# Kernel tuning notes

Hardware: AMD Instinct MI355X
Metric: run time of the kernel (lower is better)

Reference implementation:

```python
import jax, jax.numpy as jnp
import numpy as np

N_VERTS = 200000
N_TETS = 800000
FREQ_NUM = 4
SCALE = 1.0
HID = 256
D_IN = 3 + 6 * FREQ_NUM  # 27

_TRI_TABLE = np.array([
    [-1,-1,-1,-1,-1,-1],[1,0,2,-1,-1,-1],[4,0,3,-1,-1,-1],[1,4,2,1,3,4],
    [3,1,5,-1,-1,-1],[2,3,0,2,5,3],[1,4,0,1,5,4],[4,2,5,-1,-1,-1],
    [4,5,2,-1,-1,-1],[4,1,0,4,5,1],[3,2,0,3,5,2],[1,3,5,-1,-1,-1],
    [4,1,2,4,3,1],[3,0,4,-1,-1,-1],[2,0,1,-1,-1,-1],[-1,-1,-1,-1,-1,-1]], dtype=np.int32)
_NUM_TRI = np.array([0,1,1,2,1,2,2,1,1,2,2,1,2,1,1,0], dtype=np.int32)
_BASE_EDGES = np.array([0,1,0,2,0,3,1,2,1,3,2,3], dtype=np.int32)


def _pos_enc(x):
    feats = [x]
    for i in range(FREQ_NUM):
        f = float(2 ** i) * np.pi / SCALE
        feats.append(jnp.sin(f * x))
        feats.append(jnp.cos(f * x))
    return jnp.concatenate(feats, axis=-1)  # [N, 27]


def _mlp_sdf(pos, w0, b0, w1, b1, w2, b2, w3, b3, wf, bf):
    h = jax.nn.relu(_pos_enc(pos) @ w0 + b0)
    for w, b in ((w1, b1), (w2, b2), (w3, b3)):
        h = jax.nn.relu(h @ w + b)
    return (h @ wf + bf)[:, 0]  # [N]


def setup_inputs() -> dict:
    key = jax.random.key(0)
    ks = jax.random.split(key, 12)
    def lin(k, fan_in, shape):
        return jax.random.normal(k, shape, jnp.float32) * (2.0 / fan_in) ** 0.5
    return {
        "pos": jax.random.normal(ks[0], (N_VERTS, 3), jnp.float32),
        "tet_fx4": jax.random.randint(ks[1], (N_TETS, 4), 0, N_VERTS, dtype=jnp.int32),
        "w0": lin(ks[2], D_IN, (D_IN, HID)), "b0": jnp.zeros((HID,), jnp.float32),
        "w1": lin(ks[3], HID, (HID, HID)), "b1": jnp.zeros((HID,), jnp.float32),
        "w2": lin(ks[4], HID, (HID, HID)), "b2": jnp.zeros((HID,), jnp.float32),
        "w3": lin(ks[5], HID, (HID, HID)), "b3": jnp.zeros((HID,), jnp.float32),
        "wf": lin(ks[6], HID, (HID, 1)), "bf": jnp.zeros((1,), jnp.float32),
    }


def reference(pos, tet_fx4, w0, b0, w1, b1, w2, b2, w3, b3, wf, bf):
    # SDF from the positional-encoding MLP (DMTetGeometry)
    sdf = _mlp_sdf(pos, w0, b0, w1, b1, w2, b2, w3, b3, wf, bf)

    # --- marching tetrahedra (DMTet.__call__) ---
    occ = sdf > 0                       # [N]
    occ_fx4 = occ[tet_fx4]              # [F,4]
    occ_sum = occ_fx4.sum(-1)
    valid = (occ_sum > 0) & (occ_sum < 4)
    vt = tet_fx4[valid]                 # [V,4] tets crossed by the surface
    occ_v = occ_fx4[valid]              # [V,4]

    # all 6 edges per valid tet, sorted so (lo, hi)
    e = vt[:, _BASE_EDGES].reshape(-1, 2)                         # [6V,2]
    e = jnp.stack([jnp.minimum(e[:, 0], e[:, 1]),
                   jnp.maximum(e[:, 0], e[:, 1])], axis=1)
    uniq, inv = jnp.unique(e, axis=0, return_inverse=True)        # dedup edges
    inv = inv.reshape(-1)

    # edges whose endpoints straddle the zero level set
    cross = occ[uniq].sum(-1) == 1                                 # [U]
    mapping = jnp.where(cross, jnp.cumsum(cross) - 1, -1)          # compact ids
    idx_map = mapping[inv].reshape(-1, 6)                          # [V,6]
    interp_v = uniq[cross]                                         # [M,2]

    # linear interpolation of crossing vertices along each crossing edge
    p = pos[interp_v]                                              # [M,2,3]
    s = sdf[interp_v]                                              # [M,2]
    denom = s[:, 0] - s[:, 1]                                      # s0 + (-s1)
    verts = (p[:, 0] * (-s[:, 1])[:, None] + p[:, 1] * s[:, 0][:, None]) / denom[:, None]

    # triangle table lookup
    tetindex = (occ_v.astype(jnp.int32) * (2 ** jnp.arange(4, dtype=jnp.int32))).sum(-1)
    ntri = jnp.asarray(_NUM_TRI)[tetindex]
    tri = jnp.asarray(_TRI_TABLE)[tetindex]
    m1 = ntri == 1
    m2 = ntri == 2
    f1 = jnp.take_along_axis(idx_map[m1], tri[m1][:, :3], axis=1).reshape(-1, 3)
    f2 = jnp.take_along_axis(idx_map[m2], tri[m2][:, :6], axis=1).reshape(-1, 3)
    faces = jnp.concatenate([f1, f2], axis=0)
    return verts, faces
```

## Files before the change

### kernel.cpp

```cpp
#include <hip/hip_runtime.h>
#include <cstdint>
#include <cstddef>

#define NV 200000
#define NT 800000
#define ROWS 64
#define MAINB 3072
#define TAILB 212
#define MBLK (MAINB+TAILB)
#define NBLK 3125
#define NSEGS 196
#define PCAP 4096

typedef unsigned int u32;
typedef unsigned long long u64;

typedef __attribute__((ext_vector_type(8))) _Float16 half8;
typedef __attribute__((ext_vector_type(4))) float f32x4;
#define MFMA16F __builtin_amdgcn_mfma_f32_16x16x32_f16

__constant__ int c_tri[16][6] = {
  {-1,-1,-1,-1,-1,-1},{1,0,2,-1,-1,-1},{4,0,3,-1,-1,-1},{1,4,2,1,3,4},
  {3,1,5,-1,-1,-1},{2,3,0,2,5,3},{1,4,0,1,5,4},{4,2,5,-1,-1,-1},
  {4,5,2,-1,-1,-1},{4,1,0,4,5,1},{3,2,0,3,5,2},{1,3,5,-1,-1,-1},
  {4,1,2,4,3,1},{3,0,4,-1,-1,-1},{2,0,1,-1,-1,-1},{-1,-1,-1,-1,-1,-1}};
__constant__ int c_ntri[16] = {0,1,1,2,1,2,2,1,1,2,2,1,2,1,1,0};
__constant__ int c_be[12] = {0,1,0,2,0,3,1,2,1,3,2,3};

__device__ __forceinline__ void split2(float x, _Float16& h, _Float16& m){
  h = (_Float16)x;
  const float r = x - (float)h;
  m = (_Float16)(r * 2048.0f);
}

__global__ void split_weights(const float* __restrict__ w0, const float* __restrict__ w1,
                              const float* __restrict__ w2, const float* __restrict__ w3,
                              _Float16* __restrict__ wp, u32* __restrict__ segcur)
{
  const int idx = blockIdx.x*256 + threadIdx.x;
  if (idx < 256) segcur[idx] = 0u;
  int base, k, n, psz;
  float val;
  if (idx < 8192){
    base = 0; psz = 8192; k = idx >> 8; n = idx & 255;
    val = (k < 27) ? w0[k*256 + n] : 0.f;
  } else {
    int r = idx - 8192;
    const int l = r >> 16;
    r &= 65535;
    k = r >> 8; n = r & 255; psz = 65536;
    base = 16384 + l*131072;
    const float* w = (l==0) ? w1 : (l==1) ? w2 : w3;
    val = w[k*256 + n];
  }
  _Float16 h, m; split2(val, h, m);
  const int c = k >> 5, kk = k & 31;
  const int off = (c*256 + n)*32 + kk;
  wp[base + off] = h;
  wp[base + psz + off] = m;
}

template<int MT, int NC, bool LAST>
__device__ __forceinline__ void layer_run(
    const _Float16* __restrict__ Wl, const float* __restrict__ Bv,
    const float* __restrict__ wfv,
    _Float16* __restrict__ Af, float (*part)[8],
    int lane, int wv)
{
  const int l15 = lane & 15, q = lane >> 4;
  const int col0 = wv * 32;
  constexpr u32 PSTl = (u32)(MT*16*264);
  f32x4 g0[MT][2], g1[MT][2];
#pragma unroll
  for (int i=0;i<MT;i++)
#pragma unroll
    for (int j=0;j<2;j++){ g0[i][j] = (f32x4){0.f,0.f,0.f,0.f}; g1[i][j] = (f32x4){0.f,0.f,0.f,0.f}; }

  const _Float16* bp = Wl + (u32)((col0 + l15)*32 + q*8);
  half8 bA[2][2], bB[2][2];

  auto loadB = [&](int c, half8 (*dst)[2]){
#pragma unroll
    for (int p=0;p<2;p++)
#pragma unroll
      for (int nt=0;nt<2;nt++)
        dst[p][nt] = *(const half8*)(bp + (p*NC + c)*8192 + nt*512);
  };
  auto compute = [&](int c, const half8 (*bb)[2]){
#pragma unroll
    for (int mt=0;mt<MT;mt++){
      const _Float16* ap = Af + (u32)((mt*16 + l15)*264 + c*32 + q*8);
      const half8 ah = *(const half8*)(ap);
      const half8 am = *(const half8*)(ap + PSTl);
#pragma unroll
      for (int nt=0;nt<2;nt++){
        g0[mt][nt] = MFMA16F(ah, bb[0][nt], g0[mt][nt], 0,0,0);
        g1[mt][nt] = MFMA16F(ah, bb[1][nt], g1[mt][nt], 0,0,0);
        g1[mt][nt] = MFMA16F(am, bb[0][nt], g1[mt][nt], 0,0,0);
      }
    }
  };

  loadB(0, bA);
  if (NC == 1){
    compute(0, bA);
  } else {
#pragma unroll 1
    for (int ch=0; ch<NC/2; ch++){
      const int c0 = 2*ch;
      loadB(c0+1, bB);
      compute(c0, bA);
      if (c0+2 < NC) loadB(c0+2, bA);
      compute(c0+1, bB);
    }
  }
  __syncthreads();

  const float S = 4.8828125e-4f;
  if (!LAST){
#pragma unroll
    for (int nt=0;nt<2;nt++){
      const int col = col0 + nt*16 + l15;
      const float bias = Bv[col];
#pragma unroll
      for (int mt=0;mt<MT;mt++)
#pragma unroll
        for (int reg=0;reg<4;reg++){
          const int row = mt*16 + q*4 + reg;
          const float v = fmaxf(g0[mt][nt][reg] + S*g1[mt][nt][reg] + bias, 0.f);
          _Float16 h,m; split2(v,h,m);
          Af[(u32)(row*264 + col)] = h;
          Af[PSTl + (u32)(row*264 + col)] = m;
        }
    }
  } else {
    float pr[MT][4];
#pragma unroll
    for (int mt=0;mt<MT;mt++)
#pragma unroll
      for (int reg=0;reg<4;reg++) pr[mt][reg] = 0.f;
#pragma unroll
    for (int nt=0;nt<2;nt++){
      const int col = col0 + nt*16 + l15;
      const float bias = Bv[col];
      const float w = wfv[col];
#pragma unroll
      for (int mt=0;mt<MT;mt++)
#pragma unroll
        for (int reg=0;reg<4;reg++)
          pr[mt][reg] += fmaxf(g0[mt][nt][reg] + S*g1[mt][nt][reg] + bias, 0.f) * w;
    }
#pragma unroll
    for (int s=1;s<16;s<<=1)
#pragma unroll
      for (int mt=0;mt<MT;mt++)
#pragma unroll
        for (int reg=0;reg<4;reg++)
          pr[mt][reg] += __shfl_xor(pr[mt][reg], s, 64);
    if (l15 == 0){
#pragma unroll
      for (int mt=0;mt<MT;mt++)
#pragma unroll
        for (int reg=0;reg<4;reg++)
          part[mt*16 + q*4 + reg][wv] = pr[mt][reg];
    }
  }
  __syncthreads();
}

__device__ __forceinline__ float posenc_val(const float* __restrict__ pos, int gr, int f){
  if (f < 3) return pos[gr*3 + f];
  if (f < 27){
    const int g = (f-3)/6, rem = (f-3)%6;
    const int d = rem % 3;
    const float x = pos[gr*3 + d];
    const float fr = (float)(1 << g) * 3.14159265358979323846f;
    return (rem < 3) ? sinf(fr*x) : cosf(fr*x);
  }
  return 0.f;
}

__global__ __launch_bounds__(512,4) void mlp_mfma(
    const float* __restrict__ pos, const _Float16* __restrict__ wp,
    const float* __restrict__ b0, const float* __restrict__ b1,
    const float* __restrict__ b2, const float* __restrict__ b3,
    const float* __restrict__ wf, const float* __restrict__ bf,
    float* __restrict__ sdf)
{
  __shared__ _Float16 Af[2*ROWS*264];
  __shared__ float part[ROWS][8];
  const int tid = threadIdx.x;
  const int lane = tid & 63, wv = tid >> 6;
  const int bid = blockIdx.x;

  if (bid < MAINB){
    const int row0 = bid * ROWS;
#pragma unroll
    for (int it=0; it<4; it++){
      const int idx = it*512 + tid;
      const int r = idx & 63, f = idx >> 6;
      const float val = posenc_val(pos, row0 + r, f);
      _Float16 h,m; split2(val,h,m);
      Af[(u32)(r*264 + f)] = h;
      Af[(u32)(ROWS*264 + r*264 + f)] = m;
    }
    __syncthreads();

    layer_run<4,1,false>(wp + 0,      b0, nullptr, Af, part, lane, wv);
    layer_run<4,8,false>(wp + 16384,  b1, nullptr, Af, part, lane, wv);
    layer_run<4,8,false>(wp + 147456, b2, nullptr, Af, part, lane, wv);
    layer_run<4,8,true >(wp + 278528, b3, wf,      Af, part, lane, wv);

    if (tid < ROWS){
      float s = 0.f;
#pragma unroll
      for (int w=0; w<8; w++) s += part[tid][w];
      sdf[row0 + tid] = s + bf[0];
    }
  } else {
    const int row0 = MAINB*ROWS + (bid - MAINB) * 16;
    {
      const int r = tid & 15, f = tid >> 4;
      const float val = posenc_val(pos, row0 + r, f);
      _Float16 h,m; split2(val,h,m);
      Af[(u32)(r*264 + f)] = h;
      Af[(u32)(16*264 + r*264 + f)] = m;
    }
    __syncthreads();

    layer_run<1,1,false>(wp + 0,      b0, nullptr, Af, part, lane, wv);
    layer_run<1,8,false>(wp + 16384,  b1, nullptr, Af, part, lane, wv);
    layer_run<1,8,false>(wp + 147456, b2, nullptr, Af, part, lane, wv);
    layer_run<1,8,true >(wp + 278528, b3, wf,      Af, part, lane, wv);

    if (tid < 16){
      float s = 0.f;
#pragma unroll
      for (int w=0; w<8; w++) s += part[tid][w];
      sdf[row0 + tid] = s + bf[0];
    }
  }
}

__device__ __forceinline__ u32 wave_scan_incl(u32 v, int lane){
#pragma unroll
  for (int s=1;s<64;s<<=1){
    const u32 y = __shfl_up(v, s, 64);
    if (lane >= s) v += y;
  }
  return v;
}
__device__ __forceinline__ u32 block_scan_fast(u32 v, u32* sh4, int tid){
  const int lane = tid & 63, wv = tid >> 6;
  const u32 incl = wave_scan_incl(v, lane);
  if (lane == 63) sh4[wv] = incl;
  __syncthreads();
  u32 base = 0;
#pragma unroll
  for (int w=0;w<3;w++) if (w < wv) base += sh4[w];
  return incl + base;
}
__device__ __forceinline__ u64 bscan_u64(u64 v, u64* sh, int tid){
  sh[tid]=v; __syncthreads();
#pragma unroll
  for (int s=1;s<256;s<<=1){
    const u64 y = (tid>=s) ? sh[tid-s] : 0ull;
    __syncthreads();
    sh[tid] += y;
    __syncthreads();
  }
  return sh[tid];
}

__global__ void tet_pairs(const int* __restrict__ tet, const float* __restrict__ sdf,
    unsigned char* __restrict__ codes, u32* __restrict__ tscan, u32* __restrict__ tsum,
    u32* __restrict__ segcur, u64* __restrict__ pairs)
{
  __shared__ u32 sh4[4];
  const int tid = threadIdx.x;
  const int t = blockIdx.x*256 + tid;
  const int4 v = *(const int4*)(&tet[4*t]);
  const int o0 = sdf[v.x] > 0.f;
  const int o1 = sdf[v.y] > 0.f;
  const int o2 = sdf[v.z] > 0.f;
  const int o3 = sdf[v.w] > 0.f;
  const int code = o0 | (o1<<1) | (o2<<2) | (o3<<3);
  codes[t] = (unsigned char)code;
  const int nt = c_ntri[code];
  if (nt > 0){
    const int vv[4] = {v.x, v.y, v.z, v.w};
    const int oc[4] = {o0,o1,o2,o3};
#pragma unroll
    for (int e=0;e<6;e++){
      const int ia = c_be[2*e], ib = c_be[2*e+1];
      if (oc[ia] != oc[ib]){
        const int p = vv[ia], q = vv[ib];
        const int lo = p<q ? p : q, hi = p<q ? q : p;
        const int seg = lo >> 10;
        const u32 slot = atomicAdd(&segcur[seg], 1u);
        if (slot < PCAP)
          pairs[(size_t)seg*PCAP + slot] = ((u64)(u32)lo << 32) | (u32)hi;
      }
    }
  }
  const u32 my = (u32)(nt==1) | ((u32)(nt==2)<<16);
  const u32 incl = block_scan_fast(my, sh4, tid);
  tscan[t] = incl - my;
  if (tid == 255) tsum[blockIdx.x] = incl;
}

__global__ void seg_process(const u64* __restrict__ pairs_in, const u32* __restrict__ segcur,
    u64* __restrict__ uq, u32* __restrict__ ucnt, u32* __restrict__ ucnt_ex,
    u32* __restrict__ usum, const u32* __restrict__ tsum, u64* __restrict__ tsumE,
    u32* __restrict__ meta)
{
  const int tid = threadIdx.x;
  if (blockIdx.x == NSEGS){
    __shared__ u64 sh64[256];
    u64 loc[13]; u64 tot = 0ull;
#pragma unroll
    for (int i=0;i<13;i++){
      const int idx = tid*13 + i;
      const u32 p = (idx < NBLK) ? tsum[idx] : 0u;
      const u64 u = (u64)(p & 0xffffu) | ((u64)(p >> 16) << 32);
      loc[i] = u; tot += u;
    }
    const u64 incl = bscan_u64(tot, sh64, tid);
    u64 run = incl - tot;
#pragma unroll
    for (int i=0;i<13;i++){
      const int idx = tid*13 + i;
      if (idx < NBLK) tsumE[idx] = run;
      run += loc[i];
    }
    if (tid == 255){ meta[0] = (u32)(incl & 0xffffffffull); meta[1] = (u32)(incl >> 32); }
    return;
  }

  __shared__ u64 P[PCAP];
  __shared__ u32 sh4[4];
  __shared__ u32 shbase;
  const int seg = blockIdx.x;
  int n = (int)segcur[seg];
  if (n > PCAP) n = PCAP;
  int np = 1; while (np < n) np <<= 1;

  for (int i=tid; i<np; i+=256)
    P[i] = (i < n) ? pairs_in[(size_t)seg*PCAP + i] : ~0ull;
  if (tid == 0) shbase = 0u;
  __syncthreads();

  for (int k=2; k<=np; k<<=1){
    for (int j=k>>1; j>0; j>>=1){
      for (int i=tid; i<np; i+=256){
        const int ij = i ^ j;
        if (ij > i){
          const u64 a = P[i], b = P[ij];
          const bool up = ((i & k) == 0);
          if ((a > b) == up){ P[i] = b; P[ij] = a; }
        }
      }
      __syncthreads();
    }
  }

  for (int c=0; c<n; c+=256){
    const int i = c + tid;
    u64 key = 0ull; u32 f = 0u;
    if (i < n){
      key = P[i];
      f = (i == 0 || P[i] != P[i-1]) ? 1u : 0u;
    }
    __syncthreads();
    const u32 incl = block_scan_fast(f, sh4, tid);
    const u32 base = shbase;
    if (f) P[base + incl - 1u] = key;
    __syncthreads();
    if (tid == 255) shbase = base + incl;
    __syncthreads();
  }
  const int uc = (int)shbase;

  for (int i=tid; i<uc; i+=256) uq[(size_t)seg*PCAP + i] = P[i];

  const int lo0 = seg << 10;
  for (int c=0; c<1024; c+=256){
    const int lo = lo0 + c + tid;
    if (lo < NV){
      const u64 kl = (u64)(u32)lo << 32;
      const u64 kh = (u64)(u32)(lo+1) << 32;
      int a=0, b=uc;
      while (a < b){ const int m=(a+b)>>1; if (P[m] < kl) a=m+1; else b=m; }
      const int lb = a;
      b = uc;
      while (a < b){ const int m=(a+b)>>1; if (P[m] < kh) a=m+1; else b=m; }
      ucnt_ex[lo] = (u32)lb;
      ucnt[lo] = (u32)(a - lb);
    }
  }
  if (tid == 0) usum[seg] = (u32)uc;
}

__global__ void emit_all(const int* __restrict__ tet, const float* __restrict__ pos,
    const float* __restrict__ sdf, const unsigned char* __restrict__ codes,
    const u32* __restrict__ tscan, const u64* __restrict__ tsumE, const u32* __restrict__ meta,
    const u64* __restrict__ uq, const u32* __restrict__ ucnt, const u32* __restrict__ ucnt_ex,
    const u32* __restrict__ usum, float* __restrict__ out, int out_size)
{
  __shared__ u32 sh4[4];
  __shared__ u32 shu[NSEGS];
  __shared__ u32 shM;
  const int tid = threadIdx.x;
  {
    const u32 v = (tid < NSEGS) ? usum[tid] : 0u;
    const u32 incl = block_scan_fast(v, sh4, tid);
    if (tid < NSEGS) shu[tid] = incl - v;
    if (tid == NSEGS-1) shM = incl;
    __syncthreads();
  }

  if (blockIdx.x < NSEGS){
    const int seg = blockIdx.x;
    const int uc = (int)usum[seg];
    const u32 base = shu[seg];
    for (int i=tid; i<uc; i+=256){
      const u64 key = uq[(size_t)seg*PCAP + i];
      const int lo = (int)(key >> 32);
      const int hi = (int)(key & 0xffffffffull);
      const float s0 = sdf[lo], s1 = sdf[hi];
      const float d = s0 - s1;
      const float vx = (pos[3*lo  ]*(-s1) + pos[3*hi  ]*s0) / d;
      const float vy = (pos[3*lo+1]*(-s1) + pos[3*hi+1]*s0) / d;
      const float vz = (pos[3*lo+2]*(-s1) + pos[3*hi+2]*s0) / d;
      const long long w = 3ll*(long long)(base + (u32)i);
      if (w + 3 <= (long long)out_size){
        out[w] = vx; out[w+1] = vy; out[w+2] = vz;
      }
    }
  } else {
    const int t = (blockIdx.x - NSEGS)*256 + tid;
    const int code = codes[t];
    const int nt = c_ntri[code];
    if (nt == 0) return;
    const u64 tb = tsumE[t>>8];
    const u32 ts = tscan[t];
    const u32 n1e = (u32)(tb & 0xffffffffull) + (ts & 0xffffu);
    const u32 n2e = (u32)(tb >> 32) + (ts >> 16);
    const u32 N1 = meta[0];
    const u32 M  = shM;
    const u32 fb = (nt==1) ? n1e : (N1 + 2u*n2e);
    const int4 v = *(const int4*)(&tet[4*t]);
    const int vv[4] = {v.x, v.y, v.z, v.w};
    for (int r=0;r<nt;r++){
      for (int k=0;k<3;k++){
        const int e = c_tri[code][3*r+k];
        const int ia = c_be[2*e], ib = c_be[2*e+1];
        const int p = vv[ia], q = vv[ib];
        const int lo = p<q ? p : q, hi = p<q ? q : p;
        const int seg = lo >> 10;
        const u32 st = ucnt_ex[lo];
        const int u = (int)ucnt[lo];
        const u64* b = uq + (size_t)seg*PCAP + st;
        int id = -1;
        for (int j=0;j<u;j++){
          if ((int)(b[j] & 0xffffffffull) == hi){ id = (int)(shu[seg] + st) + j; break; }
        }
        const long long w = 3ll*(long long)M + 3ll*(long long)(fb + (u32)r) + k;
        if (w < (long long)out_size && id >= 0) out[w] = (float)id;
      }
    }
  }
}

extern "C" void kernel_launch(void* const* d_in, const int* in_sizes, int n_in,
                              void* d_out, int out_size, void* d_ws, size_t ws_size,
                              hipStream_t stream)
{
  (void)in_sizes; (void)n_in; (void)ws_size;
  const float* pos = (const float*)d_in[0];
  const int*   tet = (const int*)d_in[1];
  const float* w0 = (const float*)d_in[2];
  const float* b0 = (const float*)d_in[3];
  const float* w1 = (const float*)d_in[4];
  const float* b1 = (const float*)d_in[5];
  const float* w2 = (const float*)d_in[6];
  const float* b2 = (const float*)d_in[7];
  const float* w3 = (const float*)d_in[8];
  const float* b3 = (const float*)d_in[9];
  const float* wf = (const float*)d_in[10];
  const float* bf = (const float*)d_in[11];
  float* out = (float*)d_out;
  char* ws = (char*)d_ws;

  float*         sdf   = (float*)(ws + 0);
  unsigned char* codes = (unsigned char*)(ws + 800000);
  u32* tscan   = (u32*)(ws + 1600000);
  u32* tsum    = (u32*)(ws + 4800000);
  u64* tsumE   = (u64*)(ws + 4812800);
  u32* segcur  = (u32*)(ws + 4837888);
  u32* usum    = (u32*)(ws + 4838912);
  u32* meta    = (u32*)(ws + 4839936);
  u32* ucnt    = (u32*)(ws + 4840000);
  u32* ucnt_ex = (u32*)(ws + 5640000);
  _Float16* wp = (_Float16*)(ws + 6440000);
  u64* pairs   = (u64*)(ws + 7259200);

  split_weights<<<800,256,0,stream>>>(w0,w1,w2,w3,wp,segcur);
  mlp_mfma<<<MBLK,512,0,stream>>>(pos,wp,b0,b1,b2,b3,wf,bf,sdf);

  tet_pairs<<<NBLK,256,0,stream>>>(tet,sdf,codes,tscan,tsum,segcur,pairs);
  seg_process<<<NSEGS+1,256,0,stream>>>(pairs,segcur,pairs,ucnt,ucnt_ex,usum,tsum,tsumE,meta);
  emit_all<<<NSEGS+NBLK,256,0,stream>>>(tet,pos,sdf,codes,tscan,tsumE,meta,
                                        pairs,ucnt,ucnt_ex,usum,out,out_size);
}
```

Before: 443.5 us.

## Fuse marching-tet stages into one persistent kernel with grid barriers

Merges the three post-MLP kernels (tet pairing, segment sort/dedup, emit) into a single persistent kernel of 1024 blocks that grid-strides over the work and synchronizes phases with atomic spin barriers. This removes two kernel launch gaps and their tail drains. The cost is spin-wait overhead and a large shared-memory footprint (the 32KB sort buffer) in every block, which limits residency. It also relies on all 1024 blocks being co-resident, or the barrier deadlocks.

Result: slower. 888.2 us (+100.3%).

```diff
diff --git a/kernel.cpp b/kernel.cpp
--- a/kernel.cpp
+++ b/kernel.cpp
@@ -11,6 +11,7 @@
 #define NBLK 3125
 #define NSEGS 196
 #define PCAP 4096
+#define FBLK 1024
 
 typedef unsigned int u32;
 typedef unsigned long long u64;
@@ -35,10 +36,12 @@
 
 __global__ void split_weights(const float* __restrict__ w0, const float* __restrict__ w1,
                               const float* __restrict__ w2, const float* __restrict__ w3,
-                              _Float16* __restrict__ wp, u32* __restrict__ segcur)
+                              _Float16* __restrict__ wp, u32* __restrict__ segcur,
+                              u32* __restrict__ bar)
 {
   const int idx = blockIdx.x*256 + threadIdx.x;
   if (idx < 256) segcur[idx] = 0u;
+  if (idx < 8) bar[idx] = 0u;
   int base, k, n, psz;
   float val;
   if (idx < 8192){
@@ -272,51 +275,71 @@
   return sh[tid];
 }
 
-__global__ void tet_pairs(const int* __restrict__ tet, const float* __restrict__ sdf,
-    unsigned char* __restrict__ codes, u32* __restrict__ tscan, u32* __restrict__ tsum,
-    u32* __restrict__ segcur, u64* __restrict__ pairs)
+__device__ __forceinline__ void gridbar(u32* bar, int idx, int tid){
+  __threadfence();
+  __syncthreads();
+  if (tid == 0){
+    __hip_atomic_fetch_add(&bar[idx], 1u, __ATOMIC_ACQ_REL, __HIP_MEMORY_SCOPE_AGENT);
+    while (__hip_atomic_load(&bar[idx], __ATOMIC_ACQUIRE, __HIP_MEMORY_SCOPE_AGENT) < (u32)FBLK)
+      __builtin_amdgcn_s_sleep(2);
+  }
+  __syncthreads();
+  __threadfence();
+}
+
+__global__ __launch_bounds__(256,4) void tet_fused(
+    const int* __restrict__ tet, const float* __restrict__ pos,
+    const float* __restrict__ sdf,
+    unsigned char* __restrict__ codes, u32* __restrict__ tscan,
+    u32* __restrict__ tsum, u32* __restrict__ segcur, u64* __restrict__ pairs,
+    u32* __restrict__ ucnt, u32* __restrict__ ucnt_ex, u32* __restrict__ usum,
+    u64* __restrict__ tsumE, u32* __restrict__ meta, u32* __restrict__ bar,
+    float* __restrict__ out, int out_size)
 {
+  __shared__ u64 P[PCAP];
+  __shared__ u64 sh64[256];
   __shared__ u32 sh4[4];
+  __shared__ u32 shbase;
+  __shared__ u32 shu[NSEGS];
+  __shared__ u32 shM;
   const int tid = threadIdx.x;
-  const int t = blockIdx.x*256 + tid;
-  const int4 v = *(const int4*)(&tet[4*t]);
-  const int o0 = sdf[v.x] > 0.f;
-  const int o1 = sdf[v.y] > 0.f;
-  const int o2 = sdf[v.z] > 0.f;
-  const int o3 = sdf[v.w] > 0.f;
-  const int code = o0 | (o1<<1) | (o2<<2) | (o3<<3);
-  codes[t] = (unsigned char)code;
-  const int nt = c_ntri[code];
-  if (nt > 0){
-    const int vv[4] = {v.x, v.y, v.z, v.w};
-    const int oc[4] = {o0,o1,o2,o3};
-#pragma unroll
-    for (int e=0;e<6;e++){
-      const int ia = c_be[2*e], ib = c_be[2*e+1];
-      if (oc[ia] != oc[ib]){
-        const int p = vv[ia], q = vv[ib];
-        const int lo = p<q ? p : q, hi = p<q ? q : p;
-        const int seg = lo >> 10;
-        const u32 slot = atomicAdd(&segcur[seg], 1u);
-        if (slot < PCAP)
-          pairs[(size_t)seg*PCAP + slot] = ((u64)(u32)lo << 32) | (u32)hi;
-      }
-    }
-  }
-  const u32 my = (u32)(nt==1) | ((u32)(nt==2)<<16);
-  const u32 incl = block_scan_fast(my, sh4, tid);
-  tscan[t] = incl - my;
-  if (tid == 255) tsum[blockIdx.x] = incl;
-}
-
-__global__ void seg_process(const u64* __restrict__ pairs_in, const u32* __restrict__ segcur,
-    u64* __restrict__ uq, u32* __restrict__ ucnt, u32* __restrict__ ucnt_ex,
-    u32* __restrict__ usum, const u32* __restrict__ tsum, u64* __restrict__ tsumE,
-    u32* __restrict__ meta)
-{
-  const int tid = threadIdx.x;
-  if (blockIdx.x == NSEGS){
-    __shared__ u64 sh64[256];
+  const int bid = blockIdx.x;
+
+  for (int tb = bid; tb < NBLK; tb += FBLK){
+    const int t = tb*256 + tid;
+    const int4 v = *(const int4*)(&tet[4*t]);
+    const int o0 = sdf[v.x] > 0.f;
+    const int o1 = sdf[v.y] > 0.f;
+    const int o2 = sdf[v.z] > 0.f;
+    const int o3 = sdf[v.w] > 0.f;
+    const int code = o0 | (o1<<1) | (o2<<2) | (o3<<3);
+    codes[t] = (unsigned char)code;
+    const int nt = c_ntri[code];
+    if (nt > 0){
+      const int vv[4] = {v.x, v.y, v.z, v.w};
+      const int oc[4] = {o0,o1,o2,o3};
+#pragma unroll
+      for (int e=0;e<6;e++){
+        const int ia = c_be[2*e], ib = c_be[2*e+1];
+        if (oc[ia] != oc[ib]){
+          const int p = vv[ia], q = vv[ib];
+          const int lo = p<q ? p : q, hi = p<q ? q : p;
+          const int seg = lo >> 10;
+          const u32 slot = atomicAdd(&segcur[seg], 1u);
+          if (slot < PCAP)
+            pairs[(size_t)seg*PCAP + slot] = ((u64)(u32)lo << 32) | (u32)hi;
+        }
+      }
+    }
+    const u32 my = (u32)(nt==1) | ((u32)(nt==2)<<16);
+    const u32 incl = block_scan_fast(my, sh4, tid);
+    tscan[t] = incl - my;
+    if (tid == 255) tsum[tb] = incl;
+    __syncthreads();
+  }
+  gridbar(bar, 0, tid);
+
+  if (bid == NSEGS){
     u64 loc[13]; u64 tot = 0ull;
 #pragma unroll
     for (int i=0;i<13;i++){
@@ -334,83 +357,69 @@
       run += loc[i];
     }
     if (tid == 255){ meta[0] = (u32)(incl & 0xffffffffull); meta[1] = (u32)(incl >> 32); }
-    return;
-  }
-
-  __shared__ u64 P[PCAP];
-  __shared__ u32 sh4[4];
-  __shared__ u32 shbase;
-  const int seg = blockIdx.x;
-  int n = (int)segcur[seg];
-  if (n > PCAP) n = PCAP;
-  int np = 1; while (np < n) np <<= 1;
-
-  for (int i=tid; i<np; i+=256)
-    P[i] = (i < n) ? pairs_in[(size_t)seg*PCAP + i] : ~0ull;
-  if (tid == 0) shbase = 0u;
-  __syncthreads();
-
-  for (int k=2; k<=np; k<<=1){
-    for (int j=k>>1; j>0; j>>=1){
-      for (int i=tid; i<np; i+=256){
-        const int ij = i ^ j;
-        if (ij > i){
-          const u64 a = P[i], b = P[ij];
-          const bool up = ((i & k) == 0);
-          if ((a > b) == up){ P[i] = b; P[ij] = a; }
+  } else if (bid < NSEGS){
+    const int seg = bid;
+    int n = (int)segcur[seg];
+    if (n > PCAP) n = PCAP;
+    int np = 1; while (np < n) np <<= 1;
+
+    for (int i=tid; i<np; i+=256)
+      P[i] = (i < n) ? pairs[(size_t)seg*PCAP + i] : ~0ull;
+    if (tid == 0) shbase = 0u;
+    __syncthreads();
+
+    for (int k=2; k<=np; k<<=1){
+      for (int j=k>>1; j>0; j>>=1){
+        for (int i=tid; i<np; i+=256){
+          const int ij = i ^ j;
+          if (ij > i){
+            const u64 a = P[i], b = P[ij];
+            const bool up = ((i & k) == 0);
+            if ((a > b) == up){ P[i] = b; P[ij] = a; }
+          }
         }
+        __syncthreads();
+      }
+    }
+
+    for (int c=0; c<n; c+=256){
+      const int i = c + tid;
+      u64 key = 0ull; u32 f = 0u;
+      if (i < n){
+        key = P[i];
+        f = (i == 0 || P[i] != P[i-1]) ? 1u : 0u;
       }
       __syncthreads();
-    }
-  }
-
-  for (int c=0; c<n; c+=256){
-    const int i = c + tid;
-    u64 key = 0ull; u32 f = 0u;
-    if (i < n){
-      key = P[i];
-      f = (i == 0 || P[i] != P[i-1]) ? 1u : 0u;
-    }
-    __syncthreads();
-    const u32 incl = block_scan_fast(f, sh4, tid);
-    const u32 base = shbase;
-    if (f) P[base + incl - 1u] = key;
-    __syncthreads();
-    if (tid == 255) shbase = base + incl;
-    __syncthreads();
-  }
-  const int uc = (int)shbase;
-
-  for (int i=tid; i<uc; i+=256) uq[(size_t)seg*PCAP + i] = P[i];
-
-  const int lo0 = seg << 10;
-  for (int c=0; c<1024; c+=256){
-    const int lo = lo0 + c + tid;
-    if (lo < NV){
-      const u64 kl = (u64)(u32)lo << 32;
-      const u64 kh = (u64)(u32)(lo+1) << 32;
-      int a=0, b=uc;
-      while (a < b){ const int m=(a+b)>>1; if (P[m] < kl) a=m+1; else b=m; }
-      const int lb = a;
-      b = uc;
-      while (a < b){ const int m=(a+b)>>1; if (P[m] < kh) a=m+1; else b=m; }
-      ucnt_ex[lo] = (u32)lb;
-      ucnt[lo] = (u32)(a - lb);
-    }
-  }
-  if (tid == 0) usum[seg] = (u32)uc;
-}
-
-__global__ void emit_all(const int* __restrict__ tet, const float* __restrict__ pos,
-    const float* __restrict__ sdf, const unsigned char* __restrict__ codes,
-    const u32* __restrict__ tscan, const u64* __restrict__ tsumE, const u32* __restrict__ meta,
-    const u64* __restrict__ uq, const u32* __restrict__ ucnt, const u32* __restrict__ ucnt_ex,
-    const u32* __restrict__ usum, float* __restrict__ out, int out_size)
-{
-  __shared__ u32 sh4[4];
-  __shared__ u32 shu[NSEGS];
-  __shared__ u32 shM;
-  const int tid = threadIdx.x;
+      const u32 incl = block_scan_fast(f, sh4, tid);
+      const u32 base = shbase;
+      if (f) P[base + incl - 1u] = key;
+      __syncthreads();
+      if (tid == 255) shbase = base + incl;
+      __syncthreads();
+    }
+    const int uc = (int)shbase;
+
+    for (int i=tid; i<uc; i+=256) pairs[(size_t)seg*PCAP + i] = P[i];
+
+    const int lo0 = seg << 10;
+    for (int c=0; c<1024; c+=256){
+      const int lo = lo0 + c + tid;
+      if (lo < NV){
+        const u64 kl = (u64)(u32)lo << 32;
+        const u64 kh = (u64)(u32)(lo+1) << 32;
+        int a=0, b=uc;
+        while (a < b){ const int m=(a+b)>>1; if (P[m] < kl) a=m+1; else b=m; }
+        const int lb = a;
+        b = uc;
+        while (a < b){ const int m=(a+b)>>1; if (P[m] < kh) a=m+1; else b=m; }
+        ucnt_ex[lo] = (u32)lb;
+        ucnt[lo] = (u32)(a - lb);
+      }
+    }
+    if (tid == 0) usum[seg] = (u32)uc;
+  }
+  gridbar(bar, 1, tid);
+
   {
     const u32 v = (tid < NSEGS) ? usum[tid] : 0u;
     const u32 incl = block_scan_fast(v, sh4, tid);
@@ -419,54 +428,57 @@
     __syncthreads();
   }
 
-  if (blockIdx.x < NSEGS){
-    const int seg = blockIdx.x;
-    const int uc = (int)usum[seg];
-    const u32 base = shu[seg];
-    for (int i=tid; i<uc; i+=256){
-      const u64 key = uq[(size_t)seg*PCAP + i];
-      const int lo = (int)(key >> 32);
-      const int hi = (int)(key & 0xffffffffull);
-      const float s0 = sdf[lo], s1 = sdf[hi];
-      const float d = s0 - s1;
-      const float vx = (pos[3*lo  ]*(-s1) + pos[3*hi  ]*s0) / d;
-      const float vy = (pos[3*lo+1]*(-s1) + pos[3*hi+1]*s0) / d;
-      const float vz = (pos[3*lo+2]*(-s1) + pos[3*hi+2]*s0) / d;
-      const long long w = 3ll*(long long)(base + (u32)i);
-      if (w + 3 <= (long long)out_size){
-        out[w] = vx; out[w+1] = vy; out[w+2] = vz;
-      }
-    }
-  } else {
-    const int t = (blockIdx.x - NSEGS)*256 + tid;
-    const int code = codes[t];
-    const int nt = c_ntri[code];
-    if (nt == 0) return;
-    const u64 tb = tsumE[t>>8];
-    const u32 ts = tscan[t];
-    const u32 n1e = (u32)(tb & 0xffffffffull) + (ts & 0xffffu);
-    const u32 n2e = (u32)(tb >> 32) + (ts >> 16);
-    const u32 N1 = meta[0];
-    const u32 M  = shM;
-    const u32 fb = (nt==1) ? n1e : (N1 + 2u*n2e);
-    const int4 v = *(const int4*)(&tet[4*t]);
-    const int vv[4] = {v.x, v.y, v.z, v.w};
-    for (int r=0;r<nt;r++){
-      for (int k=0;k<3;k++){
-        const int e = c_tri[code][3*r+k];
-        const int ia = c_be[2*e], ib = c_be[2*e+1];
-        const int p = vv[ia], q = vv[ib];
-        const int lo = p<q ? p : q, hi = p<q ? q : p;
-        const int seg = lo >> 10;
-        const u32 st = ucnt_ex[lo];
-        const int u = (int)ucnt[lo];
-        const u64* b = uq + (size_t)seg*PCAP + st;
-        int id = -1;
-        for (int j=0;j<u;j++){
-          if ((int)(b[j] & 0xffffffffull) == hi){ id = (int)(shu[seg] + st) + j; break; }
+  for (int tb = bid; tb < NSEGS + NBLK; tb += FBLK){
+    if (tb < NSEGS){
+      const int seg = tb;
+      const int uc = (int)usum[seg];
+      const u32 base = shu[seg];
+      for (int i=tid; i<uc; i+=256){
+        const u64 key = pairs[(size_t)seg*PCAP + i];
+        const int lo = (int)(key >> 32);
+        const int hi = (int)(key & 0xffffffffull);
+        const float s0 = sdf[lo], s1 = sdf[hi];
+        const float d = s0 - s1;
+        const float vx = (pos[3*lo  ]*(-s1) + pos[3*hi  ]*s0) / d;
+        const float vy = (pos[3*lo+1]*(-s1) + pos[3*hi+1]*s0) / d;
+        const float vz = (pos[3*lo+2]*(-s1) + pos[3*hi+2]*s0) / d;
+        const long long w = 3ll*(long long)(base + (u32)i);
+        if (w + 3 <= (long long)out_size){
+          out[w] = vx; out[w+1] = vy; out[w+2] = vz;
         }
-        const long long w = 3ll*(long long)M + 3ll*(long long)(fb + (u32)r) + k;
-        if (w < (long long)out_size && id >= 0) out[w] = (float)id;
+      }
+    } else {
+      const int t = (tb - NSEGS)*256 + tid;
+      const int code = codes[t];
+      const int nt = c_ntri[code];
+      if (nt > 0){
+        const u64 tb64 = tsumE[t>>8];
+        const u32 ts = tscan[t];
+        const u32 n1e = (u32)(tb64 & 0xffffffffull) + (ts & 0xffffu);
+        const u32 n2e = (u32)(tb64 >> 32) + (ts >> 16);
+        const u32 N1 = meta[0];
+        const u32 M  = shM;
+        const u32 fb = (nt==1) ? n1e : (N1 + 2u*n2e);
+        const int4 v = *(const int4*)(&tet[4*t]);
+        const int vv[4] = {v.x, v.y, v.z, v.w};
+        for (int r=0;r<nt;r++){
+          for (int k=0;k<3;k++){
+            const int e = c_tri[code][3*r+k];
+            const int ia = c_be[2*e], ib = c_be[2*e+1];
+            const int p = vv[ia], q = vv[ib];
+            const int lo = p<q ? p : q, hi = p<q ? q : p;
+            const int seg = lo >> 10;
+            const u32 st = ucnt_ex[lo];
+            const int u = (int)ucnt[lo];
+            const u64* b = pairs + (size_t)seg*PCAP + st;
+            int id = -1;
+            for (int j=0;j<u;j++){
+              if ((int)(b[j] & 0xffffffffull) == hi){ id = (int)(shu[seg] + st) + j; break; }
+            }
+            const long long w = 3ll*(long long)M + 3ll*(long long)(fb + (u32)r) + k;
+            if (w < (long long)out_size && id >= 0) out[w] = (float)id;
+          }
+        }
       }
     }
   }
@@ -500,16 +512,14 @@
   u32* segcur  = (u32*)(ws + 4837888);
   u32* usum    = (u32*)(ws + 4838912);
   u32* meta    = (u32*)(ws + 4839936);
+  u32* bar     = (u32*)(ws + 4839968);
   u32* ucnt    = (u32*)(ws + 4840000);
   u32* ucnt_ex = (u32*)(ws + 5640000);
   _Float16* wp = (_Float16*)(ws + 6440000);
   u64* pairs   = (u64*)(ws + 7259200);
 
-  split_weights<<<800,256,0,stream>>>(w0,w1,w2,w3,wp,segcur);
+  split_weights<<<800,256,0,stream>>>(w0,w1,w2,w3,wp,segcur,bar);
   mlp_mfma<<<MBLK,512,0,stream>>>(pos,wp,b0,b1,b2,b3,wf,bf,sdf);
-
-  tet_pairs<<<NBLK,256,0,stream>>>(tet,sdf,codes,tscan,tsum,segcur,pairs);
-  seg_process<<<NSEGS+1,256,0,stream>>>(pairs,segcur,pairs,ucnt,ucnt_ex,usum,tsum,tsumE,meta);
-  emit_all<<<NSEGS+NBLK,256,0,stream>>>(tet,pos,sdf,codes,tscan,tsumE,meta,
-                                        pairs,ucnt,ucnt_ex,usum,out,out_size);
-}
+  tet_fused<<<FBLK,256,0,stream>>>(tet,pos,sdf,codes,tscan,tsum,segcur,pairs,
+                                   ucnt,ucnt_ex,usum,tsumE,meta,bar,out,out_size);
+}
```
